# Optimization experiments

Hardware: AMD Instinct MI355X
Metric: run time of the kernel (lower is better)

Reference implementation:

```python
import jax, jax.numpy as jnp
import numpy as np

PI = float(np.pi)


def _conv3x3(x, w):
    # Per-sample complex 3x3 conv (torch cross-correlation, padding=1).
    # x: [B,Cin,H,W] complex64, w: [B,Cout,Cin,3,3] complex64 -> [B,Cout,H,W]
    B, Cin, H, W = x.shape
    xp = jnp.pad(x, ((0, 0), (0, 0), (1, 1), (1, 1)))
    patches = jnp.stack([xp[:, :, i:i + H, j:j + W] for i in range(3) for j in range(3)], axis=2)  # [B,Cin,9,H,W]
    return jnp.einsum('bcphw,bocp->bohw', patches, w.reshape(B, w.shape[1], Cin, 9))


def _wH(w):
    # transpose(-4,-3).transpose(-2,-1).conj() from FNS.forward
    return jnp.conj(jnp.swapaxes(jnp.swapaxes(w, 1, 2), -2, -1))


def _fns_correction(r, w1, w2, w3, wt):
    # FNS.forward: odd symmetric extension -> ifft2 -> fftshift crop -> conv chain
    # -> theta multiply -> adjoint conv chain -> pad -> ifftshift -> fft2 -> crop.
    B, C, M, N = r.shape
    N2 = 2 * (N + 1)
    rsym = jnp.zeros((B, C, N2, N2), dtype=r.dtype)
    rsym = rsym.at[:, :, 1:M + 1, 1:N + 1].set(r)
    rsym = rsym.at[:, :, M + 2:, 1:N + 1].set(-r[:, :, ::-1, :])
    rsym = rsym.at[:, :, 1:M + 1, N + 2:].set(-r[:, :, :, ::-1])
    rsym = rsym.at[:, :, M + 2:, N + 2:].set(r[:, :, ::-1, ::-1])
    rh = jnp.fft.fftshift(jnp.fft.ifft2(rsym, axes=(2, 3)), axes=(2, 3))
    lo, hi = N2 // 2 - N2 // 4, N2 // 2 + N2 // 4 + 1
    rh = rh[:, :, lo:hi, lo:hi]  # [B,1,257,257] for N=256
    rh = _conv3x3(_conv3x3(_conv3x3(rh, w1), w2), w3)
    out = rh * wt
    out = _conv3x3(_conv3x3(_conv3x3(out, _wH(w3)), _wH(w2)), _wH(w1))
    pl = N2 // 4 + 1
    pr = N2 - N2 // 2 - pl
    out = jnp.pad(out, ((0, 0), (0, 0), (pl, pr), (pl, pr)))
    out = jnp.fft.ifftshift(out, axes=(2, 3))
    e = jnp.fft.fft2(out, axes=(2, 3))
    return e[:, :, :N, :N]


def _matvec(x, kappa2, h, omega):
    # Helmholtz.matvec with Robin BC padding and 5-point Laplacian (SL=False).
    B, C, n, m = x.shape
    bc = 2.0 * h * 1j * omega
    xx = jnp.zeros((B, C, n + 2, m + 2), dtype=x.dtype)
    xx = xx.at[:, :, 1:n + 1, 1:m + 1].set(x)
    xx = xx.at[:, :, 0, 1:m + 1].set(x[:, :, 1, :] + bc * x[:, :, 0, :])
    xx = xx.at[:, :, 1:n + 1, 0].set(x[:, :, :, 1] + bc * x[:, :, :, 0])
    xx = xx.at[:, :, n + 1, 1:m + 1].set(x[:, :, -2, :] + bc * x[:, :, -1, :])
    xx = xx.at[:, :, 1:n + 1, m + 1].set(x[:, :, :, -2] + bc * x[:, :, :, -1])
    Dx = (4.0 * xx[:, :, 1:-1, 1:-1] - xx[:, :, :-2, 1:-1] - xx[:, :, 2:, 1:-1]
          - xx[:, :, 1:-1, :-2] - xx[:, :, 1:-1, 2:]) / (h * h)
    return Dx - (omega * omega) * kappa2 * x


def _forward(f, kappa, w1, w2, w3, wt, epoch):
    N = kappa.shape[-2]
    omega = {128: 20.0, 256: 40.0}.get(N, 80.0) * PI
    h = 1.0 / (N - 1)
    kappa2 = (kappa * kappa).astype(jnp.complex64)
    Dinv = 1.0 / (4.0 / (h * h) - (omega * omega) * kappa2)
    x = jnp.zeros_like(f)
    K = (epoch - 1) // 40 + 1
    for _ in range(K):
        for _ in range(3):  # Jacobi smoother, M=3, w=2/3
            x = x + (2.0 / 3.0) * Dinv * (f - _matvec(x, kappa2, h, omega))
        r = f - _matvec(x, kappa2, h, omega)
        x = x + _fns_correction(r, w1, w2, w3, wt)
    res = jnp.linalg.norm(f - _matvec(x, kappa2, h, omega), axis=(2, 3))
    return jnp.mean(res) / jnp.mean(jnp.linalg.norm(f, axis=(2, 3)))


def setup_inputs() -> dict:
    key = jax.random.key(0)
    ks = jax.random.split(key, 11)
    B, N = 8, 256
    KS = 2 * ((2 * (N + 1)) // 4) + 1  # 257 spectral crop size
    sc = 0.1
    return {
        'f_real': jax.random.normal(ks[0], (B, 1, N, N), jnp.float32),
        'f_imag': jax.random.normal(ks[1], (B, 1, N, N), jnp.float32),
        'kappa': jax.random.uniform(ks[2], (B, 1, N, N), jnp.float32, 0.5, 1.0),
        'w1_real': sc * jax.random.normal(ks[3], (B, 4, 1, 3, 3), jnp.float32),
        'w1_imag': sc * jax.random.normal(ks[4], (B, 4, 1, 3, 3), jnp.float32),
        'w2_real': sc * jax.random.normal(ks[5], (B, 4, 4, 3, 3), jnp.float32),
        'w2_imag': sc * jax.random.normal(ks[6], (B, 4, 4, 3, 3), jnp.float32),
        'w3_real': sc * jax.random.normal(ks[7], (B, 1, 4, 3, 3), jnp.float32),
        'w3_imag': sc * jax.random.normal(ks[8], (B, 1, 4, 3, 3), jnp.float32),
        'wt_real': sc * jax.random.normal(ks[9], (B, 1, KS, KS), jnp.float32),
        'wt_imag': sc * jax.random.normal(ks[10], (B, 1, KS, KS), jnp.float32),
        'epoch': 81,
    }


def reference(f_real, f_imag, kappa, w1_real, w1_imag, w2_real, w2_imag, w3_real, w3_imag, wt_real, wt_imag, epoch):
    f = (f_real + 1j * f_imag).astype(jnp.complex64)
    w1 = (w1_real + 1j * w1_imag).astype(jnp.complex64)
    w2 = (w2_real + 1j * w2_imag).astype(jnp.complex64)
    w3 = (w3_real + 1j * w3_imag).astype(jnp.complex64)
    wt = (wt_real + 1j * wt_imag).astype(jnp.complex64)
    return _forward(f, kappa, w1, w2, w3, wt, int(epoch))
```

## Files before the change

kernel.cpp:

```cpp
#include <hip/hip_runtime.h>


#define BB 8
#define NN 65536
#define MM 66049

constexpr double PI_D    = 3.14159265358979323846;
constexpr double OMEGA_D = 40.0 * PI_D;
constexpr double H_D     = 1.0 / 255.0;
constexpr float  OMEGA2F = (float)(OMEGA_D * OMEGA_D);
constexpr float  BCVF    = (float)(2.0 * H_D * OMEGA_D);
constexpr float  INVH2F  = 65025.0f;
constexpr float  C1F     = (float)(-4.0 / (514.0 * 514.0));
constexpr float  TP514   = (float)(2.0 * PI_D / 514.0);

typedef __attribute__((ext_vector_type(8))) short short8v;
typedef __attribute__((ext_vector_type(8))) unsigned short us8;
typedef __attribute__((ext_vector_type(4))) float f32x4;

__device__ inline unsigned short bfh(float x) {
    unsigned u = __float_as_uint(x);
    unsigned r = (u + 0x7FFFu + ((u >> 16) & 1u)) >> 16;
    return (unsigned short)r;
}
__device__ inline float bfh_f(unsigned short h) {
    return __uint_as_float(((unsigned)h) << 16);
}
__device__ inline void bsplit(float x, unsigned short& h, unsigned short& l) {
    h = bfh(x);
    l = bfh(x - bfh_f(h));
}

__global__ void k_init(const float* __restrict__ kappa, float* __restrict__ kap2,
                       float* __restrict__ dinv, float* __restrict__ x0,
                       float* __restrict__ acc) {
    int t = blockIdx.x * 256 + threadIdx.x;
    if (t < BB * NN) {
        float k = kappa[t];
        float k2 = k * k;
        kap2[t] = k2;
        dinv[t] = 1.0f / (4.0f * INVH2F - OMEGA2F * k2);
        x0[2 * t] = 0.f; x0[2 * t + 1] = 0.f;
    }
    if (t < 16) acc[t] = 0.f;
}

__global__ void k_mats(float* __restrict__ S, float* __restrict__ W) {
    int t = blockIdx.x * 256 + threadIdx.x;
    if (t >= 257 * 257) return;
    int i = t / 257, j = t % 257;
    if (j < 256) {
        int a = (i - 128) * (j + 1);
        int m = ((a % 514) + 514) % 514;
        S[i * 256 + j] = sinf(m * TP514);
    }
    if (i < 256) {
        int tt = (i * (j + 129)) % 514;
        float cc = cosf(tt * TP514), ss = sinf(tt * TP514);
        float sg = (i & 1) ? -1.f : 1.f;
        W[(i * 257 + j) * 2] = sg * cc;
        W[(i * 257 + j) * 2 + 1] = -sg * ss;
    }
}

__global__ void k_packstat(const float* __restrict__ S, const float* __restrict__ W,
        unsigned short* sA1h, unsigned short* sA1l,
        unsigned short* sA2h, unsigned short* sA2l,
        unsigned short* wA1h, unsigned short* wA1l,
        unsigned short* wA2h, unsigned short* wA2l,
        unsigned short* wBh,  unsigned short* wBl) {
    int t = blockIdx.x * 256 + threadIdx.x;
    if (t >= 256 * 576) return;
    int i = t / 576, c = t % 576;
    {
        unsigned short h1 = 0, l1 = 0, h2 = 0, l2 = 0, hb = 0, lb = 0;
        if (c < 514) {
            int u = c >> 1;
            float wr = W[(i * 257 + u) * 2];
            float wi = W[(i * 257 + u) * 2 + 1];
            if ((c & 1) == 0) {
                bsplit(wr, h1, l1); bsplit(wi, h2, l2); bsplit(wr, hb, lb);
            } else {
                bsplit(-wi, h1, l1); bsplit(wr, h2, l2); bsplit(wi, hb, lb);
            }
        }
        size_t o = (size_t)i * 576 + c;
        wA1h[o] = h1; wA1l[o] = l1;
        wA2h[o] = h2; wA2l[o] = l2;
        wBh[o] = hb;  wBl[o] = lb;
    }
    if (i < 129 && c < 512) {
        int m = c >> 1;
        float s = S[i * 256 + m];
        unsigned short hs, ls;
        bsplit(s, hs, ls);
        size_t o = (size_t)i * 512 + c;
        if ((c & 1) == 0) { sA1h[o] = hs; sA1l[o] = ls; sA2h[o] = 0; sA2l[o] = 0; }
        else              { sA1h[o] = 0;  sA1l[o] = 0;  sA2h[o] = hs; sA2l[o] = ls; }
    }
}

__global__ void k_stepR(const float* __restrict__ xin,
                        const float* __restrict__ fr, const float* __restrict__ fi,
                        const float* __restrict__ kap2, float* __restrict__ acc) {
    int t = blockIdx.x * 256 + threadIdx.x;
    int b = t >> 16;
    int ij = t & 65535;
    int i = ij >> 8, j = ij & 255;
    const float* xb = xin + (size_t)b * NN * 2;
    float xcr = xb[2 * ij], xci = xb[2 * ij + 1];
    float ur, ui, dr, di, lr, li, rr, ri;
    if (i > 0) { int n = ij - 256; ur = xb[2 * n]; ui = xb[2 * n + 1]; }
    else { int n = 256 + j; ur = xb[2 * n] - BCVF * xci; ui = xb[2 * n + 1] + BCVF * xcr; }
    if (i < 255) { int n = ij + 256; dr = xb[2 * n]; di = xb[2 * n + 1]; }
    else { int n = 254 * 256 + j; dr = xb[2 * n] - BCVF * xci; di = xb[2 * n + 1] + BCVF * xcr; }
    if (j > 0) { int n = ij - 1; lr = xb[2 * n]; li = xb[2 * n + 1]; }
    else { int n = i * 256 + 1; lr = xb[2 * n] - BCVF * xci; li = xb[2 * n + 1] + BCVF * xcr; }
    if (j < 255) { int n = ij + 1; rr = xb[2 * n]; ri = xb[2 * n + 1]; }
    else { int n = i * 256 + 254; rr = xb[2 * n] - BCVF * xci; ri = xb[2 * n + 1] + BCVF * xcr; }
    float k2 = kap2[t];
    float axr = (4.f * xcr - ur - dr - lr - rr) * INVH2F - OMEGA2F * k2 * xcr;
    float axi = (4.f * xci - ui - di - li - ri) * INVH2F - OMEGA2F * k2 * xci;
    float fvr = fr[t], fvi = fi[t];
    float resr = fvr - axr, resi = fvi - axi;
    float sr = resr * resr + resi * resi;
    float sf = fvr * fvr + fvi * fvi;
    for (int off = 32; off > 0; off >>= 1) {
        sr += __shfl_down(sr, off);
        sf += __shfl_down(sf, off);
    }
    __shared__ float ssr[4], ssf[4];
    int tid = threadIdx.x;
    int wid = tid >> 6, lane = tid & 63;
    if (lane == 0) { ssr[wid] = sr; ssf[wid] = sf; }
    __syncthreads();
    if (tid == 0) {
        atomicAdd(&acc[2 * b], ssr[0] + ssr[1] + ssr[2] + ssr[3]);
        atomicAdd(&acc[2 * b + 1], ssf[0] + ssf[1] + ssf[2] + ssf[3]);
    }
}

template<int RESID>
__global__ __launch_bounds__(256) void k_step2(
        const float* __restrict__ xin, float* __restrict__ xout, float* __restrict__ rb,
        const float* __restrict__ fr, const float* __restrict__ fi,
        const float* __restrict__ kap2, const float* __restrict__ dinv) {
    const int b = blockIdx.y;
    const int tx = blockIdx.x & 7, ty = blockIdx.x >> 3;
    const int x0 = tx * 32, y0 = ty * 8;
    __shared__ float2 xs[12][37];
    __shared__ float2 ys[10][35];
    __shared__ float2 fs[10][35];
    __shared__ float ks2[10][35], ds2[10][35];
    const int tid = threadIdx.x;
    const float2* xb = (const float2*)xin + (size_t)b * NN;
    for (int i = tid; i < 432; i += 256) {
        int r = i / 36, c = i % 36;
        int gy = y0 - 2 + r, gx = x0 - 2 + c;
        float2 v = make_float2(0.f, 0.f);
        if ((unsigned)gy < 256u && (unsigned)gx < 256u) v = xb[gy * 256 + gx];
        xs[r][c] = v;
    }
    for (int i = tid; i < 340; i += 256) {
        int r = i / 34, c = i % 34;
        int gy = y0 - 1 + r, gx = x0 - 1 + c;
        float2 fv = make_float2(0.f, 0.f); float kv = 0.f, dvv = 0.f;
        if ((unsigned)gy < 256u && (unsigned)gx < 256u) {
            size_t o = (size_t)b * NN + gy * 256 + gx;
            fv = make_float2(fr[o], fi[o]); kv = kap2[o]; dvv = dinv[o];
        }
        fs[r][c] = fv; ks2[r][c] = kv; ds2[r][c] = dvv;
    }
    __syncthreads();
    for (int i = tid; i < 340; i += 256) {
        int r = i / 34, c = i % 34;
        int gy = y0 - 1 + r, gx = x0 - 1 + c;
        float2 o = make_float2(0.f, 0.f);
        if ((unsigned)gy < 256u && (unsigned)gx < 256u) {
            int xr = r + 1, xc = c + 1;
            float2 ctr = xs[xr][xc];
            float2 up, dn, lf, rt;
            if (gy > 0) up = xs[xr - 1][xc];
            else { float2 n = xs[xr + 1][xc]; up = make_float2(n.x - BCVF * ctr.y, n.y + BCVF * ctr.x); }
            if (gy < 255) dn = xs[xr + 1][xc];
            else { float2 n = xs[xr - 1][xc]; dn = make_float2(n.x - BCVF * ctr.y, n.y + BCVF * ctr.x); }
            if (gx > 0) lf = xs[xr][xc - 1];
            else { float2 n = xs[xr][xc + 1]; lf = make_float2(n.x - BCVF * ctr.y, n.y + BCVF * ctr.x); }
            if (gx < 255) rt = xs[xr][xc + 1];
            else { float2 n = xs[xr][xc - 1]; rt = make_float2(n.x - BCVF * ctr.y, n.y + BCVF * ctr.x); }
            float k2 = ks2[r][c];
            float axr = (4.f * ctr.x - up.x - dn.x - lf.x - rt.x) * INVH2F - OMEGA2F * k2 * ctr.x;
            float axi = (4.f * ctr.y - up.y - dn.y - lf.y - rt.y) * INVH2F - OMEGA2F * k2 * ctr.y;
            float2 fv = fs[r][c];
            float dv = ds2[r][c] * (2.0f / 3.0f);
            o = make_float2(ctr.x + dv * (fv.x - axr), ctr.y + dv * (fv.y - axi));
        }
        ys[r][c] = o;
    }
    __syncthreads();
    const int lx = tid & 31, ly = tid >> 5;
    const int gy = y0 + ly, gx = x0 + lx;
    const int yr = ly + 1, yc = lx + 1;
    float2 ctr = ys[yr][yc];
    float2 up, dn, lf, rt;
    if (gy > 0) up = ys[yr - 1][yc];
    else { float2 n = ys[yr + 1][yc]; up = make_float2(n.x - BCVF * ctr.y, n.y + BCVF * ctr.x); }
    if (gy < 255) dn = ys[yr + 1][yc];
    else { float2 n = ys[yr - 1][yc]; dn = make_float2(n.x - BCVF * ctr.y, n.y + BCVF * ctr.x); }
    if (gx > 0) lf = ys[yr][yc - 1];
    else { float2 n = ys[yr][yc + 1]; lf = make_float2(n.x - BCVF * ctr.y, n.y + BCVF * ctr.x); }
    if (gx < 255) rt = ys[yr][yc + 1];
    else { float2 n = ys[yr][yc - 1]; rt = make_float2(n.x - BCVF * ctr.y, n.y + BCVF * ctr.x); }
    float k2 = ks2[yr][yc];
    float axr = (4.f * ctr.x - up.x - dn.x - lf.x - rt.x) * INVH2F - OMEGA2F * k2 * ctr.x;
    float axi = (4.f * ctr.y - up.y - dn.y - lf.y - rt.y) * INVH2F - OMEGA2F * k2 * ctr.y;
    float2 fv = fs[yr][yc];
    size_t t = (size_t)b * NN + gy * 256 + gx;
    if (!RESID) {
        float dv = ds2[yr][yc] * (2.0f / 3.0f);
        xout[2 * t] = ctr.x + dv * (fv.x - axr);
        xout[2 * t + 1] = ctr.y + dv * (fv.y - axi);
    } else {
        xout[2 * t] = ctr.x; xout[2 * t + 1] = ctr.y;
        rb[2 * t] = fv.x - axr; rb[2 * t + 1] = fv.y - axi;
    }
}

__global__ __launch_bounds__(256) void k_packT(
        const float* __restrict__ in, int Min, int Nin, int KP,
        long inStrF2, unsigned short* __restrict__ Bh, unsigned short* __restrict__ Bl,
        long outStr) {
    int b = blockIdx.z;
    int n0 = blockIdx.x * 32, u0 = blockIdx.y * 32;
    __shared__ float2 lds[32][33];
    int tid = threadIdx.x;
    int r = tid >> 5, c = tid & 31;
    const float2* ip = (const float2*)in + (size_t)b * inStrF2;
    for (int rr = r; rr < 32; rr += 8) {
        int u = u0 + rr, n = n0 + c;
        float2 v = make_float2(0.f, 0.f);
        if (u < Min && n < Nin) v = ip[(size_t)u * Nin + n];
        lds[rr][c] = v;
    }
    __syncthreads();
    int tn = tid >> 3, tu4 = (tid & 7) * 4;
    int n = n0 + tn;
    if (n >= Nin) return;
    if (u0 + tu4 + 4 > (KP >> 1)) return;
    unsigned short hs[8], ls[8];
#pragma unroll
    for (int j = 0; j < 4; j++) {
        float2 v = lds[tu4 + j][tn];
        bsplit(v.x, hs[2 * j], ls[2 * j]);
        bsplit(v.y, hs[2 * j + 1], ls[2 * j + 1]);
    }
    size_t o = (size_t)b * outStr + (size_t)n * KP + 2 * (u0 + tu4);
    *(ushort4*)&Bh[o]     = make_ushort4(hs[0], hs[1], hs[2], hs[3]);
    *(ushort4*)&Bh[o + 4] = make_ushort4(hs[4], hs[5], hs[6], hs[7]);
    *(ushort4*)&Bl[o]     = make_ushort4(ls[0], ls[1], ls[2], ls[3]);
    *(ushort4*)&Bl[o + 4] = make_ushort4(ls[4], ls[5], ls[6], ls[7]);
}

template<int EPI>
__global__ __launch_bounds__(256) void mgemm(
        const unsigned short* __restrict__ A1h, const unsigned short* __restrict__ A1l,
        const unsigned short* __restrict__ A2h, const unsigned short* __restrict__ A2l,
        const unsigned short* __restrict__ Bh,  const unsigned short* __restrict__ Bl,
        float* __restrict__ C,
        unsigned short* __restrict__ P1h, unsigned short* __restrict__ P1l,
        unsigned short* __restrict__ P2h, unsigned short* __restrict__ P2l,
        int M, int N, int KP, int ldc, int KPout,
        long aStr, long bStr, long cStrF2, long pStr, float scale) {
    constexpr int LR = 72;
    __shared__ unsigned short shA1h[32 * LR], shA1l[32 * LR];
    __shared__ unsigned short shA2h[32 * LR], shA2l[32 * LR];
    __shared__ unsigned short shBh[32 * LR], shBl[32 * LR];
    const int tid = threadIdx.x;
    const int b = blockIdx.z;
    const unsigned short* pA1h = A1h + (size_t)b * aStr;
    const unsigned short* pA1l = A1l + (size_t)b * aStr;
    const unsigned short* pA2h = A2h + (size_t)b * aStr;
    const unsigned short* pA2l = A2l + (size_t)b * aStr;
    const unsigned short* pBh  = Bh + (size_t)b * bStr;
    const unsigned short* pBl  = Bl + (size_t)b * bStr;
    const int m0 = blockIdx.y * 32, n0 = blockIdx.x * 32;
    const int wave = tid >> 6, lane = tid & 63;
    const int wm = wave >> 1, wn = wave & 1;
    const int srow = tid >> 3, scol = (tid & 7) * 8;

    f32x4 accr = {0.f, 0.f, 0.f, 0.f}, acci = {0.f, 0.f, 0.f, 0.f};
    const int nks = KP >> 6;
    for (int ks = 0; ks < nks; ks++) {
        const int kb = ks * 64;
        const int so = srow * LR + scol;
        {
            int gm = m0 + srow;
            if (gm < M) {
                size_t ao = (size_t)gm * KP + kb + scol;
                *(us8*)&shA1h[so] = *(const us8*)&pA1h[ao];
                *(us8*)&shA1l[so] = *(const us8*)&pA1l[ao];
                *(us8*)&shA2h[so] = *(const us8*)&pA2h[ao];
                *(us8*)&shA2l[so] = *(const us8*)&pA2l[ao];
            } else {
                us8 z = (us8)0;
                *(us8*)&shA1h[so] = z; *(us8*)&shA1l[so] = z;
                *(us8*)&shA2h[so] = z; *(us8*)&shA2l[so] = z;
            }
            int gn = n0 + srow;
            if (gn < N) {
                size_t bo = (size_t)gn * KP + kb + scol;
                *(us8*)&shBh[so] = *(const us8*)&pBh[bo];
                *(us8*)&shBl[so] = *(const us8*)&pBl[bo];
            } else {
                us8 z = (us8)0;
                *(us8*)&shBh[so] = z; *(us8*)&shBl[so] = z;
            }
        }
        __syncthreads();
#pragma unroll
        for (int half = 0; half < 2; half++) {
            const int ko = half * 32 + ((lane >> 4) << 3);
            const int ar = (wm * 16 + (lane & 15)) * LR + ko;
            const int br = (wn * 16 + (lane & 15)) * LR + ko;
            short8v a1h = *(const short8v*)&shA1h[ar];
            short8v a1l = *(const short8v*)&shA1l[ar];
            short8v a2h = *(const short8v*)&shA2h[ar];
            short8v a2l = *(const short8v*)&shA2l[ar];
            short8v bh  = *(const short8v*)&shBh[br];
            short8v bl  = *(const short8v*)&shBl[br];
            accr = __builtin_amdgcn_mfma_f32_16x16x32_bf16(a1h, bh, accr, 0, 0, 0);
            accr = __builtin_amdgcn_mfma_f32_16x16x32_bf16(a1l, bh, accr, 0, 0, 0);
            accr = __builtin_amdgcn_mfma_f32_16x16x32_bf16(a1h, bl, accr, 0, 0, 0);
            acci = __builtin_amdgcn_mfma_f32_16x16x32_bf16(a2h, bh, acci, 0, 0, 0);
            acci = __builtin_amdgcn_mfma_f32_16x16x32_bf16(a2l, bh, acci, 0, 0, 0);
            acci = __builtin_amdgcn_mfma_f32_16x16x32_bf16(a2h, bl, acci, 0, 0, 0);
        }
        __syncthreads();
    }
    const int col = n0 + wn * 16 + (lane & 15);
    const int rbase = m0 + wm * 16 + ((lane >> 4) << 2);
    if (EPI == 3) {
        unsigned short* q1h = P1h + (size_t)b * pStr;
        unsigned short* q1l = P1l + (size_t)b * pStr;
        unsigned short* q2h = P2h + (size_t)b * pStr;
        unsigned short* q2l = P2l + (size_t)b * pStr;
#pragma unroll
        for (int i = 0; i < 4; i++) {
            int row = rbase + i;
            if (row >= M || col >= N) continue;
            float vr = scale * accr[i], vi = scale * acci[i];
            unsigned short hr, lr2, hi2, li2;
            bsplit(vr, hr, lr2); bsplit(vi, hi2, li2);
            size_t o = (size_t)row * KPout + 2 * col;
            q1h[o] = hr;  q1h[o + 1] = hi2 ^ 0x8000;
            q1l[o] = lr2; q1l[o + 1] = li2 ^ 0x8000;
            q2h[o] = hi2; q2h[o + 1] = hr;
            q2l[o] = li2; q2l[o + 1] = lr2;
        }
    } else {
        float* Cb = C + (size_t)b * cStrF2 * 2;
#pragma unroll
        for (int i = 0; i < 4; i++) {
            int row = rbase + i;
            if (row >= M || col >= N) continue;
            float vr = scale * accr[i], vi = scale * acci[i];
            if (EPI == 2) {
                int mm = 256 - row, nm = 256 - col;
                Cb[((size_t)row * 257 + col) * 2] = vr;  Cb[((size_t)row * 257 + col) * 2 + 1] = vi;
                Cb[((size_t)mm * 257 + col) * 2] = -vr;  Cb[((size_t)mm * 257 + col) * 2 + 1] = -vi;
                Cb[((size_t)row * 257 + nm) * 2] = -vr;  Cb[((size_t)row * 257 + nm) * 2 + 1] = -vi;
                Cb[((size_t)mm * 257 + nm) * 2] = vr;    Cb[((size_t)mm * 257 + nm) * 2 + 1] = vi;
            } else {
                size_t o = ((size_t)row * ldc + col) * 2;
                if (EPI == 1) { Cb[o] += vr; Cb[o + 1] += vi; }
                else          { Cb[o] = vr;  Cb[o + 1] = vi; }
            }
        }
    }
}

template<int ADJ, int WTM>
__global__ __launch_bounds__(256) void k_convChain(
        const float* __restrict__ in, float* __restrict__ out,
        const float* __restrict__ w1r, const float* __restrict__ w1i,
        const float* __restrict__ w2r, const float* __restrict__ w2i,
        const float* __restrict__ w3r, const float* __restrict__ w3i,
        const float* __restrict__ wtr, const float* __restrict__ wti) {
    const int b = blockIdx.y;
    const int bx = blockIdx.x % 9, by = blockIdx.x / 9;
    const int x0 = bx * 32, y0 = by * 8;
    __shared__ float2 sh0[14][39];
    __shared__ float2 i1[4][12][37];
    __shared__ float2 i2[4][10][35];
    __shared__ float wAr[36], wAi[36], wBr[144], wBi[144], wCr[36], wCi[36];
    const int tid = threadIdx.x;
    if (tid < 36) {
        int o = tid / 9, pq = tid % 9, p = pq / 3, q = pq % 3;
        if (!ADJ) { int idx = b * 36 + o * 9 + pq; wAr[tid] = w1r[idx]; wAi[tid] = w1i[idx]; }
        else      { int idx = b * 36 + o * 9 + q * 3 + p; wAr[tid] = w3r[idx]; wAi[tid] = -w3i[idx]; }
    } else if (tid < 180) {
        int j = tid - 36; int o = j / 36, ci = (j / 9) & 3, pq = j % 9, p = pq / 3, q = pq % 3;
        if (!ADJ) { int idx = b * 144 + (o * 4 + ci) * 9 + pq; wBr[j] = w2r[idx]; wBi[j] = w2i[idx]; }
        else      { int idx = b * 144 + (ci * 4 + o) * 9 + q * 3 + p; wBr[j] = w2r[idx]; wBi[j] = -w2i[idx]; }
    } else if (tid < 216) {
        int j = tid - 180; int ci = j / 9, pq = j % 9, p = pq / 3, q = pq % 3;
        if (!ADJ) { int idx = b * 36 + ci * 9 + pq; wCr[j] = w3r[idx]; wCi[j] = w3i[idx]; }
        else      { int idx = b * 36 + ci * 9 + q * 3 + p; wCr[j] = w1r[idx]; wCi[j] = -w1i[idx]; }
    }
    const float2* ipb = (const float2*)in + (size_t)b * MM;
    for (int i = tid; i < 14 * 38; i += 256) {
        int r = i / 38, c = i % 38;
        int gy = y0 - 3 + r, gx = x0 - 3 + c;
        float2 v = make_float2(0.f, 0.f);
        if ((unsigned)gy < 257u && (unsigned)gx < 257u) v = ipb[(size_t)gy * 257 + gx];
        sh0[r][c] = v;
    }
    __syncthreads();
    for (int i = tid; i < 1728; i += 256) {
        int ch = i / 432, rem = i % 432, r = rem / 36, c = rem % 36;
        int gy = y0 - 2 + r, gx = x0 - 2 + c;
        float ar = 0.f, ai = 0.f;
        if ((unsigned)gy < 257u && (unsigned)gx < 257u) {
#pragma unroll
            for (int p = 0; p < 3; p++)
#pragma unroll
                for (int q = 0; q < 3; q++) {
                    float2 v = sh0[r + p][c + q];
                    float wr = wAr[ch * 9 + p * 3 + q], wi = wAi[ch * 9 + p * 3 + q];
                    ar += v.x * wr - v.y * wi;
                    ai += v.x * wi + v.y * wr;
                }
        }
        i1[ch][r][c] = make_float2(ar, ai);
    }
    __syncthreads();
    for (int i = tid; i < 1360; i += 256) {
        int ch = i / 340, rem = i % 340, r = rem / 34, c = rem % 34;
        int gy = y0 - 1 + r, gx = x0 - 1 + c;
        float ar = 0.f, ai = 0.f;
        if ((unsigned)gy < 257u && (unsigned)gx < 257u) {
#pragma unroll
            for (int ci = 0; ci < 4; ci++)
#pragma unroll
                for (int p = 0; p < 3; p++)
#pragma unroll
                    for (int q = 0; q < 3; q++) {
                        float2 v = i1[ci][r + p][c + q];
                        float wr = wBr[(ch * 4 + ci) * 9 + p * 3 + q];
                        float wi = wBi[(ch * 4 + ci) * 9 + p * 3 + q];
                        ar += v.x * wr - v.y * wi;
                        ai += v.x * wi + v.y * wr;
                    }
        }
        i2[ch][r][c] = make_float2(ar, ai);
    }
    __syncthreads();
    const int lx = tid & 31, ly = tid >> 5;
    const int x = x0 + lx, y = y0 + ly;
    if (x >= 257 || y >= 257) return;
    float ar = 0.f, ai = 0.f;
#pragma unroll
    for (int ci = 0; ci < 4; ci++)
#pragma unroll
        for (int p = 0; p < 3; p++)
#pragma unroll
            for (int q = 0; q < 3; q++) {
                float2 v = i2[ci][ly + p][lx + q];
                float wr = wCr[ci * 9 + p * 3 + q], wi = wCi[ci * 9 + p * 3 + q];
                ar += v.x * wr - v.y * wi;
                ai += v.x * wi + v.y * wr;
            }
    if (WTM) {
        size_t wo = (size_t)b * MM + (size_t)y * 257 + x;
        float wr = wtr[wo], wi = wti[wo];
        float r0 = ar * wr - ai * wi;
        float i0 = ar * wi + ai * wr;
        ar = r0; ai = i0;
    }
    ((float2*)out)[(size_t)b * MM + (size_t)y * 257 + x] = make_float2(ar, ai);
}

__global__ void k_finalize(const float* __restrict__ acc, float* __restrict__ out) {
    if (threadIdx.x == 0 && blockIdx.x == 0) {
        float num = 0.f, den = 0.f;
        for (int b = 0; b < BB; b++) {
            num += sqrtf(acc[2 * b]);
            den += sqrtf(acc[2 * b + 1]);
        }
        out[0] = num / den;
    }
}

extern "C" void kernel_launch(void* const* d_in, const int* in_sizes, int n_in,
                              void* d_out, int out_size, void* d_ws, size_t ws_size,
                              hipStream_t stream) {
    (void)in_sizes; (void)n_in; (void)out_size; (void)ws_size;
    const float* fr  = (const float*)d_in[0];
    const float* fi  = (const float*)d_in[1];
    const float* kap = (const float*)d_in[2];
    const float* w1r = (const float*)d_in[3];
    const float* w1i = (const float*)d_in[4];
    const float* w2r = (const float*)d_in[5];
    const float* w2i = (const float*)d_in[6];
    const float* w3r = (const float*)d_in[7];
    const float* w3i = (const float*)d_in[8];
    const float* wtr = (const float*)d_in[9];
    const float* wti = (const float*)d_in[10];
    const int K = 3;

    float* ws = (float*)d_ws;
    size_t off = 0;
    float* x0   = ws + off; off += (size_t)BB * NN * 2;
    float* x1   = ws + off; off += (size_t)BB * NN * 2;
    float* x2   = ws + off; off += (size_t)BB * NN * 2;
    float* rb   = ws + off; off += (size_t)BB * NN * 2;
    float* kap2 = ws + off; off += (size_t)BB * NN;
    float* dinv = ws + off; off += (size_t)BB * NN;
    float* tA   = ws + off; off += (size_t)BB * MM * 2;
    float* tB   = ws + off; off += (size_t)BB * MM * 2;
    float* u1   = ws + off; off += (size_t)BB * MM * 2;
    float* S    = ws + off; off += 257 * 256;
    float* W    = ws + off; off += 256 * 257 * 2;
    float* acc  = ws + off; off += 16;

    unsigned short* us = (unsigned short*)(ws + off);
    size_t so = 0;
    unsigned short* sA1h = us + so; so += 129 * 512;
    unsigned short* sA1l = us + so; so += 129 * 512;
    unsigned short* sA2h = us + so; so += 129 * 512;
    unsigned short* sA2l = us + so; so += 129 * 512;
    unsigned short* wA1h = us + so; so += 256 * 576;
    unsigned short* wA1l = us + so; so += 256 * 576;
    unsigned short* wA2h = us + so; so += 256 * 576;
    unsigned short* wA2l = us + so; so += 256 * 576;
    unsigned short* wBh  = us + so; so += 256 * 576;
    unsigned short* wBl  = us + so; so += 256 * 576;
    const long DSASTR = (long)129 * 512;
    unsigned short* dsA1h = us + so; so += (size_t)BB * DSASTR;
    unsigned short* dsA1l = us + so; so += (size_t)BB * DSASTR;
    unsigned short* dsA2h = us + so; so += (size_t)BB * DSASTR;
    unsigned short* dsA2l = us + so; so += (size_t)BB * DSASTR;
    const long DFASTR = (long)256 * 576;
    unsigned short* dfA1h = us + so; so += (size_t)BB * DFASTR;
    unsigned short* dfA1l = us + so; so += (size_t)BB * DFASTR;
    unsigned short* dfA2h = us + so; so += (size_t)BB * DFASTR;
    unsigned short* dfA2l = us + so; so += (size_t)BB * DFASTR;
    const long DBSTR = (long)257 * 576;
    unsigned short* dBh  = us + so; so += (size_t)BB * DBSTR;
    unsigned short* dBl  = us + so; so += (size_t)BB * DBSTR;

    int sgrid = (BB * NN + 255) / 256;
    k_init<<<sgrid, 256, 0, stream>>>(kap, kap2, dinv, x0, acc);
    k_mats<<<(257 * 257 + 255) / 256, 256, 0, stream>>>(S, W);
    k_packstat<<<(256 * 576 + 255) / 256, 256, 0, stream>>>(
        S, W, sA1h, sA1l, sA2h, sA2l, wA1h, wA1l, wA2h, wA2l, wBh, wBl);

    float* xc = x0;
    for (int it = 0; it < K; ++it) {
        float* xn = (xc == x0) ? x2 : x0;
        k_step2<0><<<dim3(256, BB), 256, 0, stream>>>(xc, x1, rb, fr, fi, kap2, dinv);
        k_step2<1><<<dim3(256, BB), 256, 0, stream>>>(x1, xn, rb, fr, fi, kap2, dinv);

        k_packT<<<dim3(8, 8, BB), 256, 0, stream>>>(rb, 256, 256, 512,
            (long)NN, dBh, dBl, DBSTR);
        mgemm<3><<<dim3(8, 5, BB), 256, 0, stream>>>(
            sA1h, sA1l, sA2h, sA2l, dBh, dBl, nullptr,
            dsA1h, dsA1l, dsA2h, dsA2l,
            129, 256, 512, 0, 512, 0, DBSTR, 0, DSASTR, 1.f);
        mgemm<2><<<dim3(5, 5, BB), 256, 0, stream>>>(
            dsA1h, dsA1l, dsA2h, dsA2l, sA1h, sA1l, tB,
            nullptr, nullptr, nullptr, nullptr,
            129, 129, 512, 257, 0, DSASTR, 0, (long)MM, 0, C1F);

        k_convChain<0, 1><<<dim3(297, BB), 256, 0, stream>>>(
            tB, u1, w1r, w1i, w2r, w2i, w3r, w3i, wtr, wti);
        k_convChain<1, 0><<<dim3(297, BB), 256, 0, stream>>>(
            u1, tA, w1r, w1i, w2r, w2i, w3r, w3i, wtr, wti);

        k_packT<<<dim3(9, 9, BB), 256, 0, stream>>>(tA, 257, 257, 576,
            (long)MM, dBh, dBl, DBSTR);
        mgemm<3><<<dim3(9, 8, BB), 256, 0, stream>>>(
            wA1h, wA1l, wA2h, wA2l, dBh, dBl, nullptr,
            dfA1h, dfA1l, dfA2h, dfA2l,
            256, 257, 576, 0, 576, 0, DBSTR, 0, DFASTR, 1.f);
        mgemm<1><<<dim3(8, 8, BB), 256, 0, stream>>>(
            dfA1h, dfA1l, dfA2h, dfA2l, wBh, wBl, xn,
            nullptr, nullptr, nullptr, nullptr,
            256, 256, 576, 256, 0, DFASTR, 0, (long)NN, 0, 1.f);
        xc = xn;
    }
    k_stepR<<<sgrid, 256, 0, stream>>>(xc, fr, fi, kap2, acc);
    k_finalize<<<1, 64, 0, stream>>>(acc, (float*)d_out);
}
```

Measured before the change: 598.2 us.

## Fuse B-operand transpose/split into GEMM loads and restructure conv chain loops

Removes the separate k_packT kernels by having the first GEMM of each transform read the float2 input directly from global memory, split it into bf16 hi/lo parts and write it transposed into shared memory. This drops two kernel launches and an intermediate buffer round-trip per iteration. The conv chain also now computes all four output channels per spatial position, which reuses each shared-memory input load across channels, and it stores the complex weights as float2. In exchange the GEMM B loads become scalar, strided, per-element shared-memory writes that may have bank conflicts, and the redundant loads now happen in every M-block.

```diff
diff --git a/kernel.cpp b/kernel.cpp
--- a/kernel.cpp
+++ b/kernel.cpp
@@ -226,46 +226,12 @@
     }
 }
 
-__global__ __launch_bounds__(256) void k_packT(
-        const float* __restrict__ in, int Min, int Nin, int KP,
-        long inStrF2, unsigned short* __restrict__ Bh, unsigned short* __restrict__ Bl,
-        long outStr) {
-    int b = blockIdx.z;
-    int n0 = blockIdx.x * 32, u0 = blockIdx.y * 32;
-    __shared__ float2 lds[32][33];
-    int tid = threadIdx.x;
-    int r = tid >> 5, c = tid & 31;
-    const float2* ip = (const float2*)in + (size_t)b * inStrF2;
-    for (int rr = r; rr < 32; rr += 8) {
-        int u = u0 + rr, n = n0 + c;
-        float2 v = make_float2(0.f, 0.f);
-        if (u < Min && n < Nin) v = ip[(size_t)u * Nin + n];
-        lds[rr][c] = v;
-    }
-    __syncthreads();
-    int tn = tid >> 3, tu4 = (tid & 7) * 4;
-    int n = n0 + tn;
-    if (n >= Nin) return;
-    if (u0 + tu4 + 4 > (KP >> 1)) return;
-    unsigned short hs[8], ls[8];
-#pragma unroll
-    for (int j = 0; j < 4; j++) {
-        float2 v = lds[tu4 + j][tn];
-        bsplit(v.x, hs[2 * j], ls[2 * j]);
-        bsplit(v.y, hs[2 * j + 1], ls[2 * j + 1]);
-    }
-    size_t o = (size_t)b * outStr + (size_t)n * KP + 2 * (u0 + tu4);
-    *(ushort4*)&Bh[o]     = make_ushort4(hs[0], hs[1], hs[2], hs[3]);
-    *(ushort4*)&Bh[o + 4] = make_ushort4(hs[4], hs[5], hs[6], hs[7]);
-    *(ushort4*)&Bl[o]     = make_ushort4(ls[0], ls[1], ls[2], ls[3]);
-    *(ushort4*)&Bl[o + 4] = make_ushort4(ls[4], ls[5], ls[6], ls[7]);
-}
-
-template<int EPI>
+template<int EPI, int BGLO>
 __global__ __launch_bounds__(256) void mgemm(
         const unsigned short* __restrict__ A1h, const unsigned short* __restrict__ A1l,
         const unsigned short* __restrict__ A2h, const unsigned short* __restrict__ A2l,
         const unsigned short* __restrict__ Bh,  const unsigned short* __restrict__ Bl,
+        const float* __restrict__ Bgf, int ldbf, long bStrG, int bMin,
         float* __restrict__ C,
         unsigned short* __restrict__ P1h, unsigned short* __restrict__ P1l,
         unsigned short* __restrict__ P2h, unsigned short* __restrict__ P2l,
@@ -281,8 +247,6 @@
     const unsigned short* pA1l = A1l + (size_t)b * aStr;
     const unsigned short* pA2h = A2h + (size_t)b * aStr;
     const unsigned short* pA2l = A2l + (size_t)b * aStr;
-    const unsigned short* pBh  = Bh + (size_t)b * bStr;
-    const unsigned short* pBl  = Bl + (size_t)b * bStr;
     const int m0 = blockIdx.y * 32, n0 = blockIdx.x * 32;
     const int wave = tid >> 6, lane = tid & 63;
     const int wm = wave >> 1, wn = wave & 1;
@@ -306,6 +270,26 @@
                 *(us8*)&shA1h[so] = z; *(us8*)&shA1l[so] = z;
                 *(us8*)&shA2h[so] = z; *(us8*)&shA2l[so] = z;
             }
+        }
+        if (BGLO) {
+            int ul = tid >> 3;
+            int nl = (tid & 7) * 4;
+            int gu = (kb >> 1) + ul;
+            const float2* bp = (const float2*)Bgf + (size_t)b * bStrG
+                               + (size_t)gu * ldbf + (n0 + nl);
+#pragma unroll
+            for (int j = 0; j < 4; j++) {
+                float2 v = make_float2(0.f, 0.f);
+                if (gu < bMin && (n0 + nl + j) < N) v = bp[j];
+                unsigned short h0, l0, h1, l1;
+                bsplit(v.x, h0, l0); bsplit(v.y, h1, l1);
+                int o = (nl + j) * LR + 2 * ul;
+                shBh[o] = h0;     shBl[o] = l0;
+                shBh[o + 1] = h1; shBl[o + 1] = l1;
+            }
+        } else {
+            const unsigned short* pBh = Bh + (size_t)b * bStr;
+            const unsigned short* pBl = Bl + (size_t)b * bStr;
             int gn = n0 + srow;
             if (gn < N) {
                 size_t bo = (size_t)gn * KP + kb + scol;
@@ -379,6 +363,7 @@
     }
 }
 
+#define CACC(AR, AI, W) { AR += v.x * (W).x - v.y * (W).y; AI += v.x * (W).y + v.y * (W).x; }
 template<int ADJ, int WTM>
 __global__ __launch_bounds__(256) void k_convChain(
         const float* __restrict__ in, float* __restrict__ out,
@@ -392,20 +377,20 @@
     __shared__ float2 sh0[14][39];
     __shared__ float2 i1[4][12][37];
     __shared__ float2 i2[4][10][35];
-    __shared__ float wAr[36], wAi[36], wBr[144], wBi[144], wCr[36], wCi[36];
+    __shared__ float2 wA2[36], wB2[144], wC2[36];
     const int tid = threadIdx.x;
     if (tid < 36) {
         int o = tid / 9, pq = tid % 9, p = pq / 3, q = pq % 3;
-        if (!ADJ) { int idx = b * 36 + o * 9 + pq; wAr[tid] = w1r[idx]; wAi[tid] = w1i[idx]; }
-        else      { int idx = b * 36 + o * 9 + q * 3 + p; wAr[tid] = w3r[idx]; wAi[tid] = -w3i[idx]; }
+        if (!ADJ) { int idx = b * 36 + o * 9 + pq; wA2[tid] = make_float2(w1r[idx], w1i[idx]); }
+        else      { int idx = b * 36 + o * 9 + q * 3 + p; wA2[tid] = make_float2(w3r[idx], -w3i[idx]); }
     } else if (tid < 180) {
         int j = tid - 36; int o = j / 36, ci = (j / 9) & 3, pq = j % 9, p = pq / 3, q = pq % 3;
-        if (!ADJ) { int idx = b * 144 + (o * 4 + ci) * 9 + pq; wBr[j] = w2r[idx]; wBi[j] = w2i[idx]; }
-        else      { int idx = b * 144 + (ci * 4 + o) * 9 + q * 3 + p; wBr[j] = w2r[idx]; wBi[j] = -w2i[idx]; }
+        if (!ADJ) { int idx = b * 144 + (o * 4 + ci) * 9 + pq; wB2[j] = make_float2(w2r[idx], w2i[idx]); }
+        else      { int idx = b * 144 + (ci * 4 + o) * 9 + q * 3 + p; wB2[j] = make_float2(w2r[idx], -w2i[idx]); }
     } else if (tid < 216) {
         int j = tid - 180; int ci = j / 9, pq = j % 9, p = pq / 3, q = pq % 3;
-        if (!ADJ) { int idx = b * 36 + ci * 9 + pq; wCr[j] = w3r[idx]; wCi[j] = w3i[idx]; }
-        else      { int idx = b * 36 + ci * 9 + q * 3 + p; wCr[j] = w1r[idx]; wCi[j] = -w1i[idx]; }
+        if (!ADJ) { int idx = b * 36 + ci * 9 + pq; wC2[j] = make_float2(w3r[idx], w3i[idx]); }
+        else      { int idx = b * 36 + ci * 9 + q * 3 + p; wC2[j] = make_float2(w1r[idx], -w1i[idx]); }
     }
     const float2* ipb = (const float2*)in + (size_t)b * MM;
     for (int i = tid; i < 14 * 38; i += 256) {
@@ -416,43 +401,54 @@
         sh0[r][c] = v;
     }
     __syncthreads();
-    for (int i = tid; i < 1728; i += 256) {
-        int ch = i / 432, rem = i % 432, r = rem / 36, c = rem % 36;
+    for (int pos = tid; pos < 432; pos += 256) {
+        int r = pos / 36, c = pos % 36;
         int gy = y0 - 2 + r, gx = x0 - 2 + c;
-        float ar = 0.f, ai = 0.f;
-        if ((unsigned)gy < 257u && (unsigned)gx < 257u) {
+        bool ok = ((unsigned)gy < 257u) & ((unsigned)gx < 257u);
+        float ar0 = 0.f, ai0 = 0.f, ar1 = 0.f, ai1 = 0.f;
+        float ar2 = 0.f, ai2 = 0.f, ar3 = 0.f, ai3 = 0.f;
+#pragma unroll
+        for (int p = 0; p < 3; p++)
+#pragma unroll
+            for (int q = 0; q < 3; q++) {
+                float2 v = sh0[r + p][c + q];
+                int k = p * 3 + q;
+                CACC(ar0, ai0, wA2[k])
+                CACC(ar1, ai1, wA2[9 + k])
+                CACC(ar2, ai2, wA2[18 + k])
+                CACC(ar3, ai3, wA2[27 + k])
+            }
+        float z = ok ? 1.f : 0.f;
+        i1[0][r][c] = make_float2(z * ar0, z * ai0);
+        i1[1][r][c] = make_float2(z * ar1, z * ai1);
+        i1[2][r][c] = make_float2(z * ar2, z * ai2);
+        i1[3][r][c] = make_float2(z * ar3, z * ai3);
+    }
+    __syncthreads();
+    for (int pos = tid; pos < 340; pos += 256) {
+        int r = pos / 34, c = pos % 34;
+        int gy = y0 - 1 + r, gx = x0 - 1 + c;
+        bool ok = ((unsigned)gy < 257u) & ((unsigned)gx < 257u);
+        float ar0 = 0.f, ai0 = 0.f, ar1 = 0.f, ai1 = 0.f;
+        float ar2 = 0.f, ai2 = 0.f, ar3 = 0.f, ai3 = 0.f;
+#pragma unroll
+        for (int ci = 0; ci < 4; ci++)
 #pragma unroll
             for (int p = 0; p < 3; p++)
 #pragma unroll
                 for (int q = 0; q < 3; q++) {
-                    float2 v = sh0[r + p][c + q];
-                    float wr = wAr[ch * 9 + p * 3 + q], wi = wAi[ch * 9 + p * 3 + q];
-                    ar += v.x * wr - v.y * wi;
-                    ai += v.x * wi + v.y * wr;
+                    float2 v = i1[ci][r + p][c + q];
+                    int k = ci * 9 + p * 3 + q;
+                    CACC(ar0, ai0, wB2[k])
+                    CACC(ar1, ai1, wB2[36 + k])
+                    CACC(ar2, ai2, wB2[72 + k])
+                    CACC(ar3, ai3, wB2[108 + k])
                 }
-        }
-        i1[ch][r][c] = make_float2(ar, ai);
-    }
-    __syncthreads();
-    for (int i = tid; i < 1360; i += 256) {
-        int ch = i / 340, rem = i % 340, r = rem / 34, c = rem % 34;
-        int gy = y0 - 1 + r, gx = x0 - 1 + c;
-        float ar = 0.f, ai = 0.f;
-        if ((unsigned)gy < 257u && (unsigned)gx < 257u) {
-#pragma unroll
-            for (int ci = 0; ci < 4; ci++)
-#pragma unroll
-                for (int p = 0; p < 3; p++)
-#pragma unroll
-                    for (int q = 0; q < 3; q++) {
-                        float2 v = i1[ci][r + p][c + q];
-                        float wr = wBr[(ch * 4 + ci) * 9 + p * 3 + q];
-                        float wi = wBi[(ch * 4 + ci) * 9 + p * 3 + q];
-                        ar += v.x * wr - v.y * wi;
-                        ai += v.x * wi + v.y * wr;
-                    }
-        }
-        i2[ch][r][c] = make_float2(ar, ai);
+        float z = ok ? 1.f : 0.f;
+        i2[0][r][c] = make_float2(z * ar0, z * ai0);
+        i2[1][r][c] = make_float2(z * ar1, z * ai1);
+        i2[2][r][c] = make_float2(z * ar2, z * ai2);
+        i2[3][r][c] = make_float2(z * ar3, z * ai3);
     }
     __syncthreads();
     const int lx = tid & 31, ly = tid >> 5;
@@ -466,9 +462,9 @@
 #pragma unroll
             for (int q = 0; q < 3; q++) {
                 float2 v = i2[ci][ly + p][lx + q];
-                float wr = wCr[ci * 9 + p * 3 + q], wi = wCi[ci * 9 + p * 3 + q];
-                ar += v.x * wr - v.y * wi;
-                ai += v.x * wi + v.y * wr;
+                float2 w = wC2[ci * 9 + p * 3 + q];
+                ar += v.x * w.x - v.y * w.y;
+                ai += v.x * w.y + v.y * w.x;
             }
     if (WTM) {
         size_t wo = (size_t)b * MM + (size_t)y * 257 + x;
@@ -545,9 +541,6 @@
     unsigned short* dfA1l = us + so; so += (size_t)BB * DFASTR;
     unsigned short* dfA2h = us + so; so += (size_t)BB * DFASTR;
     unsigned short* dfA2l = us + so; so += (size_t)BB * DFASTR;
-    const long DBSTR = (long)257 * 576;
-    unsigned short* dBh  = us + so; so += (size_t)BB * DBSTR;
-    unsigned short* dBl  = us + so; so += (size_t)BB * DBSTR;
 
     int sgrid = (BB * NN + 255) / 256;
     k_init<<<sgrid, 256, 0, stream>>>(kap, kap2, dinv, x0, acc);
@@ -561,32 +554,36 @@
         k_step2<0><<<dim3(256, BB), 256, 0, stream>>>(xc, x1, rb, fr, fi, kap2, dinv);
         k_step2<1><<<dim3(256, BB), 256, 0, stream>>>(x1, xn, rb, fr, fi, kap2, dinv);
 
-        k_packT<<<dim3(8, 8, BB), 256, 0, stream>>>(rb, 256, 256, 512,
-            (long)NN, dBh, dBl, DBSTR);
-        mgemm<3><<<dim3(8, 5, BB), 256, 0, stream>>>(
-            sA1h, sA1l, sA2h, sA2l, dBh, dBl, nullptr,
-            dsA1h, dsA1l, dsA2h, dsA2l,
-            129, 256, 512, 0, 512, 0, DBSTR, 0, DSASTR, 1.f);
-        mgemm<2><<<dim3(5, 5, BB), 256, 0, stream>>>(
-            dsA1h, dsA1l, dsA2h, dsA2l, sA1h, sA1l, tB,
-            nullptr, nullptr, nullptr, nullptr,
-            129, 129, 512, 257, 0, DSASTR, 0, (long)MM, 0, C1F);
+        mgemm<3, 1><<<dim3(8, 5, BB), 256, 0, stream>>>(
+            sA1h, sA1l, sA2h, sA2l, nullptr, nullptr,
+            rb, 256, (long)NN, 256,
+            nullptr, dsA1h, dsA1l, dsA2h, dsA2l,
+            129, 256, 512, 0, 512,
+            0, 0, 0, DSASTR, 1.f);
+        mgemm<2, 0><<<dim3(5, 5, BB), 256, 0, stream>>>(
+            dsA1h, dsA1l, dsA2h, dsA2l, sA1h, sA1l,
+            nullptr, 0, 0, 0,
+            tB, nullptr, nullptr, nullptr, nullptr,
+            129, 129, 512, 257, 0,
+            DSASTR, 0, (long)MM, 0, C1F);
 
         k_convChain<0, 1><<<dim3(297, BB), 256, 0, stream>>>(
             tB, u1, w1r, w1i, w2r, w2i, w3r, w3i, wtr, wti);
         k_convChain<1, 0><<<dim3(297, BB), 256, 0, stream>>>(
             u1, tA, w1r, w1i, w2r, w2i, w3r, w3i, wtr, wti);
 
-        k_packT<<<dim3(9, 9, BB), 256, 0, stream>>>(tA, 257, 257, 576,
-            (long)MM, dBh, dBl, DBSTR);
-        mgemm<3><<<dim3(9, 8, BB), 256, 0, stream>>>(
-            wA1h, wA1l, wA2h, wA2l, dBh, dBl, nullptr,
-            dfA1h, dfA1l, dfA2h, dfA2l,
-            256, 257, 576, 0, 576, 0, DBSTR, 0, DFASTR, 1.f);
-        mgemm<1><<<dim3(8, 8, BB), 256, 0, stream>>>(
-            dfA1h, dfA1l, dfA2h, dfA2l, wBh, wBl, xn,
-            nullptr, nullptr, nullptr, nullptr,
-            256, 256, 576, 256, 0, DFASTR, 0, (long)NN, 0, 1.f);
+        mgemm<3, 1><<<dim3(9, 8, BB), 256, 0, stream>>>(
+            wA1h, wA1l, wA2h, wA2l, nullptr, nullptr,
+            tA, 257, (long)MM, 257,
+            nullptr, dfA1h, dfA1l, dfA2h, dfA2l,
+            256, 257, 576, 0, 576,
+            0, 0, 0, DFASTR, 1.f);
+        mgemm<1, 0><<<dim3(8, 8, BB), 256, 0, stream>>>(
+            dfA1h, dfA1l, dfA2h, dfA2l, wBh, wBl,
+            nullptr, 0, 0, 0,
+            xn, nullptr, nullptr, nullptr, nullptr,
+            256, 256, 576, 256, 0,
+            DFASTR, 0, (long)NN, 0, 1.f);
         xc = xn;
     }
     k_stepR<<<sgrid, 256, 0, stream>>>(xc, fr, fi, kap2, acc);
```

New measurement: 1.596 ms. 167% more time.
